# Kernel optimization log

Hardware: AMD Instinct MI355X
Metric: run time of the kernel (lower is better)

## Reference

```python
import jax, jax.numpy as jnp
import numpy as np

ZF_MIN, ZF_MAX = 0.85, 1.15  # zoom_factor_range ('subtle and moderate')


def setup_inputs() -> dict:
    key = jax.random.key(0)
    k1, k2 = jax.random.split(key)
    image = jax.random.uniform(k1, (8, 3, 512, 512), dtype=jnp.float32)
    zoom_factor = jax.random.uniform(k2, (1,), dtype=jnp.float32)
    return {"image": image, "zoom_factor": zoom_factor, "steps": 7}


def _bilinear_sample_zeros(img, xs, ys):
    """img: [B,C,H,W]; xs, ys: [S,H,W] source pixel coords.
    Returns [B,C,S,H,W], zero padding outside the image."""
    B, C, H, W = img.shape
    x0 = jnp.floor(xs)
    y0 = jnp.floor(ys)
    wx = xs - x0  # [S,H,W]
    wy = ys - y0
    x0i = x0.astype(jnp.int32)
    y0i = y0.astype(jnp.int32)
    x1i = x0i + 1
    y1i = y0i + 1

    def gather(yi, xi):
        valid = ((xi >= 0) & (xi < W) & (yi >= 0) & (yi < H)).astype(img.dtype)
        xc = jnp.clip(xi, 0, W - 1)
        yc = jnp.clip(yi, 0, H - 1)
        # advanced indexing -> [B,C,S,H,W]
        return img[:, :, yc, xc] * valid[None, None]

    w00 = ((1.0 - wx) * (1.0 - wy))[None, None]
    w01 = (wx * (1.0 - wy))[None, None]
    w10 = ((1.0 - wx) * wy)[None, None]
    w11 = (wx * wy)[None, None]
    return (gather(y0i, x0i) * w00 + gather(y0i, x1i) * w01 +
            gather(y1i, x0i) * w10 + gather(y1i, x1i) * w11)


def reference(image, zoom_factor, steps):
    """ZoomBlur 'speed' path: per-step scale-about-center warp (kornia
    get_rotation_matrix2d with angle=0 + warp_affine, bilinear, zero pad),
    then mean over the steps dimension."""
    B, C, H, W = image.shape
    zf = ZF_MIN + (ZF_MAX - ZF_MIN) * zoom_factor[0]  # scalar final zoom
    S = int(steps)
    if S <= 1:
        return image
    # scales_i = 1 + linspace(0,1,S)_i * (zf - 1)
    interp = jnp.linspace(0.0, 1.0, S, dtype=image.dtype)  # [S]
    scales = 1.0 + interp * (zf - 1.0)                     # [S]
    cx = W / 2.0
    cy = H / 2.0
    # dst->src mapping: p_src = (p_dst - c) / s + c (inverse of scale about c)
    x = jnp.arange(W, dtype=image.dtype)  # [W]
    y = jnp.arange(H, dtype=image.dtype)  # [H]
    inv_s = 1.0 / scales  # [S]
    xs = (x[None, None, :] - cx) * inv_s[:, None, None] + cx  # [S,1,W]
    ys = (y[None, :, None] - cy) * inv_s[:, None, None] + cy  # [S,H,1]
    xs = jnp.broadcast_to(xs, (S, H, W))
    ys = jnp.broadcast_to(ys, (S, H, W))
    warped = _bilinear_sample_zeros(image, xs, ys)  # [B,C,S,H,W]
    return jnp.mean(warped, axis=2)  # [B,C,H,W]
```

## Files before the change

kernel.cpp:

```cpp
#include <hip/hip_runtime.h>

#define IW 512
#define IH 512
#define NPIX (IH * IW)
#define NK 6
#define GROUPS 8
#define PPT 3
#define LROW 520
#define GOFF 4

typedef float f4v __attribute__((ext_vector_type(4)));

struct RowTap { int rowA; float t0, t1; };

__device__ inline RowTap row_prep(float inv, float yf) {
    const float ysv = fmaf(yf, inv, 256.0f);
    const float fy  = floorf(ysv);
    const float wy  = ysv - fy;
    const int y0 = (int)fy;
    const int yb = min(max(y0, 0), IH - 2);
    const float t0 = (yb == y0 ? 1.0f - wy : 0.0f) + (yb == y0 + 1 ? wy : 0.0f);
    const float t1 = (yb + 1 == y0 ? 1.0f - wy : 0.0f) + (yb + 1 == y0 + 1 ? wy : 0.0f);
    RowTap rt;
    rt.t0 = t0 * (1.0f / 7.0f);
    rt.t1 = t1 * (1.0f / 7.0f);
    rt.rowA = yb * IW;
    return rt;
}

#define STAGE_LOAD(base_, idA_, idB_) do {                      \
    const float* __restrict__ _b = (base_);                     \
    a0 = *(const f4v*)(_b + r0.rowA + cq);                      \
    b0 = *(const f4v*)(_b + r0.rowA + IW + cq);                 \
    a1 = *(const f4v*)(_b + r1.rowA + cq);                      \
    b1 = *(const f4v*)(_b + r1.rowA + IW + cq);                 \
    a2 = *(const f4v*)(_b + r2.rowA + cq);                      \
    b2 = *(const f4v*)(_b + r2.rowA + IW + cq);                 \
    idA_ = _b[idoff];                                           \
    idB_ = _b[idoff + 256];                                     \
} while (0)

#define LERP_L() do {                                           \
    L0 = r0.t0 * a0 + r0.t1 * b0;                               \
    L1 = r1.t0 * a1 + r1.t1 * b1;                               \
    L2 = r2.t0 * a2 + r2.t1 * b2;                               \
} while (0)

#define STAGE_WRITE(B) do {                                     \
    *(f4v*)&rrow[B][woff]            = L0;                      \
    *(f4v*)&rrow[B][woff + 2 * LROW] = L1;                      \
    *(f4v*)&rrow[B][woff + 4 * LROW] = L2;                      \
} while (0)

#define COMPUTE_STORE(B, cA_, cB_, op_) do {                    \
    float aA = (cA_) * (1.0f / 7.0f);                           \
    float aB = (cB_) * (1.0f / 7.0f);                           \
    _Pragma("unroll")                                           \
    for (int k = 0; k < NK; ++k) {                              \
        const float v0A = rrow[B][offA[k]];                     \
        const float v1A = rrow[B][offA[k] + 1];                 \
        const float v0B = rrow[B][offB[k]];                     \
        const float v1B = rrow[B][offB[k] + 1];                 \
        aA = fmaf(wxA[k], v1A - v0A, aA + v0A);                 \
        aB = fmaf(wxB[k], v1B - v0B, aB + v0B);                 \
    }                                                           \
    float* _o = (op_);                                          \
    __builtin_nontemporal_store(aA, _o);                        \
    __builtin_nontemporal_store(aB, _o + 256);                  \
} while (0)

__global__ __launch_bounds__(256, 6) void zoomblur_kernel(
    const float* __restrict__ img,
    const float* __restrict__ zoomf,
    float* __restrict__ out)
{
    __shared__ float rrow[2][NK * LROW];

    const int tid   = threadIdx.x;
    const int bid   = blockIdx.x;
    const int group = bid & (GROUPS - 1);
    const int y     = bid >> 3;

    const float zf = 0.85f + 0.30f * zoomf[0];
    const float dz = zf - 1.0f;
    const float yf  = (float)y - 256.0f;
    const float xfA = (float)tid - 256.0f;
    const float xfB = (float)tid;

    float invs[NK];
#pragma unroll
    for (int s = 1; s <= NK; ++s)
        invs[s - 1] = __builtin_amdgcn_rcpf(fmaf((float)s * (1.0f / 6.0f), dz, 1.0f));

    int   offA[NK], offB[NK];
    float wxA[NK], wxB[NK];
#pragma unroll
    for (int k = 0; k < NK; ++k) {
        const float inv = invs[k];
        const float xsA = fmaf(xfA, inv, 256.0f);
        const float xsB = fmaf(xfB, inv, 256.0f);
        const float fxA = floorf(xsA);
        const float fxB = floorf(xsB);
        wxA[k] = xsA - fxA;
        wxB[k] = xsB - fxB;
        const int xA = min(max((int)fxA, -2), IW);
        const int xB = min(max((int)fxB, -2), IW);
        offA[k] = k * LROW + GOFF + xA;
        offB[k] = k * LROW + GOFF + xB;
    }

    const int sbase = tid >> 7;
    const int cq    = (tid & 127) << 2;
    const RowTap r0 = row_prep(sbase ? invs[1] : invs[0], yf);
    const RowTap r1 = row_prep(sbase ? invs[3] : invs[2], yf);
    const RowTap r2 = row_prep(sbase ? invs[5] : invs[4], yf);
    const int woff = sbase * LROW + GOFF + cq;

    if (tid < 96) {
        const int line = tid >> 3;
        const int j    = tid & 7;
        const int slot = (j < 4) ? j : 512 + j;
        const int buf  = line >= NK;
        const int l    = buf ? line - NK : line;
        rrow[buf][l * LROW + slot] = 0.0f;
    }

    const int idoff = y * IW + tid;
    const size_t pbase = (size_t)(group * PPT) * NPIX;
    const float* __restrict__ ib = img + pbase;
    float* __restrict__       ob = out + pbase;

    f4v a0, b0, a1, b1, a2, b2;
    f4v L0, L1, L2;
    float idA0, idB0, idA1, idB1, idA2, idB2;

    STAGE_LOAD(ib, idA0, idB0);
    LERP_L();
    STAGE_LOAD(ib + NPIX, idA1, idB1);
    STAGE_WRITE(0);
    __syncthreads();

    COMPUTE_STORE(0, idA0, idB0, ob + idoff);
    LERP_L();
    STAGE_LOAD(ib + 2 * NPIX, idA2, idB2);
    STAGE_WRITE(1);
    __syncthreads();

    COMPUTE_STORE(1, idA1, idB1, ob + NPIX + idoff);
    LERP_L();
    STAGE_WRITE(0);
    __syncthreads();

    COMPUTE_STORE(0, idA2, idB2, ob + 2 * NPIX + idoff);
}

extern "C" void kernel_launch(void* const* d_in, const int* in_sizes, int n_in,
                              void* d_out, int out_size, void* d_ws, size_t ws_size,
                              hipStream_t stream) {
    const float* img  = (const float*)d_in[0];
    const float* zoom = (const float*)d_in[1];
    float* out = (float*)d_out;

    dim3 block(256);
    dim3 grid(IH * GROUPS);
    zoomblur_kernel<<<grid, block, 0, stream>>>(img, zoom, out);
}
```

Measured before the change: 19.51 us.

## Single-buffer LDS row staging and raise occupancy target to 8 blocks

Drops the double-buffered shared row staging in favour of one buffer, halving LDS per block, and raises the launch-bounds minimum from 6 to 8 blocks per CU. The next plane's global loads are still issued before computing the current plane, but writes to shared memory now wait behind an extra barrier. This should allow more resident blocks and lower register pressure, at the cost of an extra __syncthreads per stage and less overlap between the LDS write and compute phases.

```diff
diff --git a/kernel.cpp b/kernel.cpp
--- a/kernel.cpp
+++ b/kernel.cpp
@@ -40,27 +40,21 @@
     idB_ = _b[idoff + 256];                                     \
 } while (0)
 
-#define LERP_L() do {                                           \
-    L0 = r0.t0 * a0 + r0.t1 * b0;                               \
-    L1 = r1.t0 * a1 + r1.t1 * b1;                               \
-    L2 = r2.t0 * a2 + r2.t1 * b2;                               \
+#define LERP_WRITE() do {                                       \
+    *(f4v*)&rrow[woff]            = r0.t0 * a0 + r0.t1 * b0;    \
+    *(f4v*)&rrow[woff + 2 * LROW] = r1.t0 * a1 + r1.t1 * b1;    \
+    *(f4v*)&rrow[woff + 4 * LROW] = r2.t0 * a2 + r2.t1 * b2;    \
 } while (0)
 
-#define STAGE_WRITE(B) do {                                     \
-    *(f4v*)&rrow[B][woff]            = L0;                      \
-    *(f4v*)&rrow[B][woff + 2 * LROW] = L1;                      \
-    *(f4v*)&rrow[B][woff + 4 * LROW] = L2;                      \
-} while (0)
-
-#define COMPUTE_STORE(B, cA_, cB_, op_) do {                    \
+#define COMPUTE_STORE(cA_, cB_, op_) do {                       \
     float aA = (cA_) * (1.0f / 7.0f);                           \
     float aB = (cB_) * (1.0f / 7.0f);                           \
     _Pragma("unroll")                                           \
     for (int k = 0; k < NK; ++k) {                              \
-        const float v0A = rrow[B][offA[k]];                     \
-        const float v1A = rrow[B][offA[k] + 1];                 \
-        const float v0B = rrow[B][offB[k]];                     \
-        const float v1B = rrow[B][offB[k] + 1];                 \
+        const float v0A = rrow[offA[k]];                        \
+        const float v1A = rrow[offA[k] + 1];                    \
+        const float v0B = rrow[offB[k]];                        \
+        const float v1B = rrow[offB[k] + 1];                    \
         aA = fmaf(wxA[k], v1A - v0A, aA + v0A);                 \
         aB = fmaf(wxB[k], v1B - v0B, aB + v0B);                 \
     }                                                           \
@@ -69,12 +63,12 @@
     __builtin_nontemporal_store(aB, _o + 256);                  \
 } while (0)
 
-__global__ __launch_bounds__(256, 6) void zoomblur_kernel(
+__global__ __launch_bounds__(256, 8) void zoomblur_kernel(
     const float* __restrict__ img,
     const float* __restrict__ zoomf,
     float* __restrict__ out)
 {
-    __shared__ float rrow[2][NK * LROW];
+    __shared__ float rrow[NK * LROW];
 
     const int tid   = threadIdx.x;
     const int bid   = blockIdx.x;
@@ -116,13 +110,11 @@
     const RowTap r2 = row_prep(sbase ? invs[5] : invs[4], yf);
     const int woff = sbase * LROW + GOFF + cq;
 
-    if (tid < 96) {
+    if (tid < 48) {
         const int line = tid >> 3;
         const int j    = tid & 7;
         const int slot = (j < 4) ? j : 512 + j;
-        const int buf  = line >= NK;
-        const int l    = buf ? line - NK : line;
-        rrow[buf][l * LROW + slot] = 0.0f;
+        rrow[line * LROW + slot] = 0.0f;
     }
 
     const int idoff = y * IW + tid;
@@ -131,27 +123,25 @@
     float* __restrict__       ob = out + pbase;
 
     f4v a0, b0, a1, b1, a2, b2;
-    f4v L0, L1, L2;
     float idA0, idB0, idA1, idB1, idA2, idB2;
 
     STAGE_LOAD(ib, idA0, idB0);
-    LERP_L();
-    STAGE_LOAD(ib + NPIX, idA1, idB1);
-    STAGE_WRITE(0);
+    LERP_WRITE();
     __syncthreads();
 
-    COMPUTE_STORE(0, idA0, idB0, ob + idoff);
-    LERP_L();
-    STAGE_LOAD(ib + 2 * NPIX, idA2, idB2);
-    STAGE_WRITE(1);
+    STAGE_LOAD(ib + NPIX, idA1, idB1);
+    COMPUTE_STORE(idA0, idB0, ob + idoff);
+    __syncthreads();
+    LERP_WRITE();
     __syncthreads();
 
-    COMPUTE_STORE(1, idA1, idB1, ob + NPIX + idoff);
-    LERP_L();
-    STAGE_WRITE(0);
+    STAGE_LOAD(ib + 2 * NPIX, idA2, idB2);
+    COMPUTE_STORE(idA1, idB1, ob + NPIX + idoff);
+    __syncthreads();
+    LERP_WRITE();
     __syncthreads();
 
-    COMPUTE_STORE(0, idA2, idB2, ob + 2 * NPIX + idoff);
+    COMPUTE_STORE(idA2, idB2, ob + 2 * NPIX + idoff);
 }
 
 extern "C" void kernel_launch(void* const* d_in, const int* in_sizes, int n_in,
```

New measurement: 20.05 us. 2.8% more time.
